# Kernel tuning notes

Hardware: AMD Instinct MI355X
Metric: run time of the kernel (lower is better)

Reference implementation:

```python
import jax, jax.numpy as jnp
import numpy as np

HEADS = 4
DIM_HEAD = 32
SCALE = DIM_HEAD ** -0.5
EPS = 1e-5


def setup_inputs() -> dict:
    key = jax.random.key(0)
    ks = jax.random.split(key, 4)
    x = jax.random.normal(ks[0], (8, 64, 32, 32, 32), dtype=jnp.float32)
    w_qkv = jax.random.normal(ks[1], (384, 64), dtype=jnp.float32) * 0.05
    w_out = jax.random.normal(ks[2], (64, 128), dtype=jnp.float32) * 0.05
    b_out = jax.random.normal(ks[3], (64,), dtype=jnp.float32) * 0.05
    gamma = jnp.ones((64,), dtype=jnp.float32)
    beta = jnp.zeros((64,), dtype=jnp.float32)
    return {"x": x, "w_qkv": w_qkv, "w_out": w_out, "b_out": b_out,
            "gamma": gamma, "beta": beta}


def reference(x, w_qkv, w_out, b_out, gamma, beta):
    b, c, l, h, w = x.shape
    n = l * h * w
    xf = x.reshape(b, c, n)
    # 1x1 Conv3d (no bias) == channel matmul
    qkv = jnp.einsum('oc,bcn->bon', w_qkv, xf)            # [b, 3*H*D, n]
    q, k, v = jnp.split(qkv, 3, axis=1)
    def to_heads(t):
        return t.reshape(b, HEADS, DIM_HEAD, n)            # [b, H, D, n]
    q, k, v = to_heads(q), to_heads(k), to_heads(v)
    q = jax.nn.softmax(q, axis=2) * SCALE                  # softmax over head dim
    k = jax.nn.softmax(k, axis=3)                          # softmax over tokens
    context = jnp.einsum('bhdn,bhen->bhde', k, v)          # [b, H, D, D]
    out = jnp.einsum('bhde,bhdn->bhen', context, q)        # [b, H, D, n]
    out = out.reshape(b, HEADS * DIM_HEAD, n)
    # to_out: 1x1 Conv3d with bias, then GroupNorm(1, dim)
    out = jnp.einsum('oc,bcn->bon', w_out, out) + b_out[None, :, None]
    mu = out.mean(axis=(1, 2), keepdims=True)
    var = out.var(axis=(1, 2), keepdims=True)
    out = (out - mu) * jax.lax.rsqrt(var + EPS)
    out = out * gamma[None, :, None] + beta[None, :, None]
    return out.reshape(b, c, l, h, w)
```

## Files before the change

### kernel.cpp

```cpp
#include <hip/hip_runtime.h>

typedef unsigned short u16;
typedef __bf16 bf16x8 __attribute__((ext_vector_type(8)));
typedef float f32x4 __attribute__((ext_vector_type(4)));
typedef short s16x4 __attribute__((ext_vector_type(4)));
typedef short s16x8 __attribute__((ext_vector_type(8)));

#define NTOK 32768
#define SCALE_F 0.17677669529663689f

__device__ __forceinline__ u16 f2bf(float f){
  unsigned u = __builtin_bit_cast(unsigned, f);
  u += 0x7fffu + ((u>>16)&1u);
  return (u16)(u>>16);
}
__device__ __forceinline__ float bf2f(u16 u){
  unsigned v = ((unsigned)u)<<16;
  return __builtin_bit_cast(float, v);
}

__global__ __launch_bounds__(256) void k1_ctx(const float* __restrict__ x,
    const float* __restrict__ wqkv, float* __restrict__ ctx, float* __restrict__ s1,
    int siters)
{
  const int b = blockIdx.y, chunk = blockIdx.x;
  const int t = threadIdx.x, w = t>>6, l = t&63, lr = l&15, lg = l>>4;
  __shared__ u16 xT[64*72];
  __shared__ u16 ek[128*72];
  __shared__ u16 vl[128*72];

  bf16x8 bw[4][2];
  #pragma unroll
  for (int ct=0;ct<4;ct++)
    #pragma unroll
    for (int ks=0;ks<2;ks++){
      const float* src = wqkv + (128 + w*64 + ct*16 + lr)*64 + ks*32 + lg*8;
      #pragma unroll
      for (int j=0;j<8;j++) ((u16*)&bw[ct][ks])[j] = f2bf(src[j]);
    }
  bf16x8 ones;
  #pragma unroll
  for (int j=0;j<8;j++) ((u16*)&ones)[j] = 0x3F80;

  f32x4 ctxa[2][2]; f32x4 s1a[2];
  #pragma unroll
  for (int i=0;i<2;i++){
    s1a[i] = f32x4{0.f,0.f,0.f,0.f};
    #pragma unroll
    for (int j=0;j<2;j++) ctxa[i][j] = f32x4{0.f,0.f,0.f,0.f};
  }
  const float* xb = x + (long)b*64*NTOK;
  u16* dst = (w<2) ? ek : vl;
  const int chb = (w&1)*64;
  const bool isk = (w<2);
  const int sn = t&63, cg = (t>>6)*16;

  float tmpf[16];
  {
    const int n0 = chunk*siters*64;
    #pragma unroll
    for (int i=0;i<16;i++) tmpf[i] = xb[(long)(cg+i)*NTOK + n0 + sn];
  }

  for (int s=0; s<siters; s++) {
    {
      u16 tmp[16];
      #pragma unroll
      for (int i=0;i<16;i++) tmp[i] = f2bf(tmpf[i]);
      *(s16x8*)&xT[sn*72 + cg]     = *(s16x8*)&tmp[0];
      *(s16x8*)&xT[sn*72 + cg + 8] = *(s16x8*)&tmp[8];
    }
    __syncthreads();
    if (s+1 < siters){
      const int n0 = (chunk*siters + s+1)*64;
      #pragma unroll
      for (int i=0;i<16;i++) tmpf[i] = xb[(long)(cg+i)*NTOK + n0 + sn];
    }
    f32x4 acc[4][4];
    #pragma unroll
    for (int rt=0;rt<4;rt++)
      #pragma unroll
      for (int ct=0;ct<4;ct++) acc[rt][ct] = f32x4{0.f,0.f,0.f,0.f};
    #pragma unroll
    for (int ks=0;ks<2;ks++){
      bf16x8 af[4];
      #pragma unroll
      for (int rt=0;rt<4;rt++)
        af[rt] = *(const bf16x8*)&xT[(rt*16+lr)*72 + ks*32 + lg*8];
      #pragma unroll
      for (int rt=0;rt<4;rt++)
        #pragma unroll
        for (int ct=0;ct<4;ct++)
          acc[rt][ct] = __builtin_amdgcn_mfma_f32_16x16x32_bf16(af[rt], bw[ct][ks], acc[rt][ct], 0,0,0);
    }
    #pragma unroll
    for (int ct=0;ct<4;ct++){
      const int row = chb + ct*16 + lr;
      #pragma unroll
      for (int rt=0;rt<4;rt++){
        s16x4 p;
        #pragma unroll
        for (int ri=0;ri<4;ri++){
          const float v = acc[rt][ct][ri];
          p[ri] = (short)f2bf(isk ? __expf(v) : v);
        }
        *(s16x4*)&dst[row*72 + rt*16 + lg*4] = p;
      }
    }
    __syncthreads();
    #pragma unroll
    for (int ks=0;ks<2;ks++){
      bf16x8 bd[2];
      #pragma unroll
      for (int cd=0;cd<2;cd++)
        bd[cd] = *(const bf16x8*)&ek[(w*32 + cd*16 + lr)*72 + ks*32 + lg*8];
      #pragma unroll
      for (int re=0;re<2;re++){
        bf16x8 a = *(const bf16x8*)&vl[(w*32 + re*16 + lr)*72 + ks*32 + lg*8];
        #pragma unroll
        for (int cd=0;cd<2;cd++)
          ctxa[re][cd] = __builtin_amdgcn_mfma_f32_16x16x32_bf16(a, bd[cd], ctxa[re][cd], 0,0,0);
      }
      #pragma unroll
      for (int cd=0;cd<2;cd++)
        s1a[cd] = __builtin_amdgcn_mfma_f32_16x16x32_bf16(ones, bd[cd], s1a[cd], 0,0,0);
    }
  }
  float* cp = ctx + ((long)b*4 + w)*1024;
  #pragma unroll
  for (int re=0;re<2;re++)
    #pragma unroll
    for (int cd=0;cd<2;cd++)
      #pragma unroll
      for (int ri=0;ri<4;ri++){
        const int e = re*16 + lg*4 + ri, d = cd*16 + lr;
        atomicAdd(&cp[e*32 + d], ctxa[re][cd][ri]);
      }
  if (lg==0){
    #pragma unroll
    for (int cd=0;cd<2;cd++)
      atomicAdd(&s1[(long)b*128 + w*32 + cd*16 + lr], s1a[cd][0]);
  }
}

__global__ __launch_bounds__(256) void k2_w2(const float* __restrict__ ctx,
    const float* __restrict__ s1, const float* __restrict__ wout, u16* __restrict__ W2)
{
  const int b = blockIdx.y, h = blockIdx.x, t = threadIdx.x;
  __shared__ float cs[1024];
  __shared__ float s1s[32];
  {
    f32x4 p4 = *(const f32x4*)(ctx + ((long)b*4 + h)*1024 + t*4);
    *(f32x4*)&cs[t*4] = p4;
  }
  if (t < 32) s1s[t] = s1[(long)b*128 + h*32 + t];
  __syncthreads();
  const int d = t & 31;
  const float rinv = SCALE_F / s1s[d];
  #pragma unroll
  for (int oi=0; oi<8; oi++){
    const int o = (t>>5)*8 + oi;
    float acc = 0.f;
    #pragma unroll
    for (int e=0;e<32;e++) acc += wout[o*128 + h*32 + e] * cs[e*32 + d];
    W2[((long)b*64 + o)*128 + h*32 + d] = f2bf(acc * rinv);
  }
}

#define K3T 4
__global__ __launch_bounds__(256) void k3_y(const float* __restrict__ x,
    const float* __restrict__ wqkv, const u16* __restrict__ W2,
    const float* __restrict__ bout, float* __restrict__ y, float* __restrict__ ysum)
{
  const int b = blockIdx.y, blk = blockIdx.x;
  const int t = threadIdx.x, w = t>>6, l = t&63, lr = l&15, lg = l>>4;
  __shared__ u16 W2s[64*136];
  __shared__ u16 xT[64*72];
  __shared__ u16 qs[64*136];
  __shared__ float red[8];
  const float* xb = x + (long)b*64*NTOK;

  bf16x8 qfr[2][2];
  #pragma unroll
  for (int rt=0;rt<2;rt++)
    #pragma unroll
    for (int ks=0;ks<2;ks++){
      const float* src = wqkv + (w*32 + rt*16 + lr)*64 + ks*32 + lg*8;
      #pragma unroll
      for (int j=0;j<8;j++) ((u16*)&qfr[rt][ks])[j] = f2bf(src[j]);
    }
  {
    const u16* src = W2 + (long)b*8192 + t*32;
    const int o = t>>2, c0 = (t&3)*32;
    #pragma unroll
    for (int k=0;k<4;k++)
      *(s16x8*)&W2s[o*136 + c0 + k*8] = *(const s16x8*)(src + k*8);
  }
  const int sn = t&63, cg = (t>>6)*16;
  float tmpf[16];
  {
    const int n0 = blk*K3T*64;
    #pragma unroll
    for (int i=0;i<16;i++) tmpf[i] = xb[(long)(cg+i)*NTOK + n0 + sn];
  }
  float sum=0.f, ss=0.f;
  float* yb = y + (long)b*64*NTOK;

  for (int ti=0; ti<K3T; ti++){
    const int n0 = (blk*K3T + ti)*64;
    {
      u16 tmp[16];
      #pragma unroll
      for (int i=0;i<16;i++) tmp[i] = f2bf(tmpf[i]);
      *(s16x8*)&xT[sn*72 + cg]     = *(s16x8*)&tmp[0];
      *(s16x8*)&xT[sn*72 + cg + 8] = *(s16x8*)&tmp[8];
    }
    __syncthreads();
    if (ti+1 < K3T){
      const int nn0 = n0 + 64;
      #pragma unroll
      for (int i=0;i<16;i++) tmpf[i] = xb[(long)(cg+i)*NTOK + nn0 + sn];
    }
    f32x4 qa[2][4];
    #pragma unroll
    for (int rt=0;rt<2;rt++)
      #pragma unroll
      for (int ct=0;ct<4;ct++) qa[rt][ct] = f32x4{0.f,0.f,0.f,0.f};
    #pragma unroll
    for (int ks=0;ks<2;ks++){
      bf16x8 bfr[4];
      #pragma unroll
      for (int ct=0;ct<4;ct++)
        bfr[ct] = *(const bf16x8*)&xT[(ct*16+lr)*72 + ks*32 + lg*8];
      #pragma unroll
      for (int rt=0;rt<2;rt++)
        #pragma unroll
        for (int ct=0;ct<4;ct++)
          qa[rt][ct] = __builtin_amdgcn_mfma_f32_16x16x32_bf16(qfr[rt][ks], bfr[ct], qa[rt][ct], 0,0,0);
    }
    #pragma unroll
    for (int ct=0;ct<4;ct++){
      float e[2][4]; float p = 0.f;
      #pragma unroll
      for (int rt=0;rt<2;rt++)
        #pragma unroll
        for (int ri=0;ri<4;ri++){ e[rt][ri] = __expf(qa[rt][ct][ri]); p += e[rt][ri]; }
      p += __shfl_xor(p, 16, 64);
      p += __shfl_xor(p, 32, 64);
      const float rinv = 1.f/p;
      const int nn = ct*16 + lr;
      #pragma unroll
      for (int rt=0;rt<2;rt++){
        s16x4 pk;
        #pragma unroll
        for (int ri=0;ri<4;ri++) pk[ri] = (short)f2bf(e[rt][ri]*rinv);
        *(s16x4*)&qs[nn*136 + w*32 + rt*16 + lg*4] = pk;
      }
    }
    __syncthreads();
    f32x4 ya[4];
    #pragma unroll
    for (int rt=0;rt<4;rt++) ya[rt] = f32x4{0.f,0.f,0.f,0.f};
    #pragma unroll
    for (int ks=0;ks<4;ks++){
      bf16x8 bq = *(const bf16x8*)&qs[(w*16+lr)*136 + ks*32 + lg*8];
      #pragma unroll
      for (int rt=0;rt<4;rt++){
        bf16x8 a = *(const bf16x8*)&W2s[(rt*16+lr)*136 + ks*32 + lg*8];
        ya[rt] = __builtin_amdgcn_mfma_f32_16x16x32_bf16(a, bq, ya[rt], 0,0,0);
      }
    }
    #pragma unroll
    for (int rt=0;rt<4;rt++)
      #pragma unroll
      for (int ri=0;ri<4;ri++){
        const int o = rt*16 + lg*4 + ri;
        const float val = ya[rt][ri] + bout[o];
        sum += val; ss += val*val;
        yb[(long)o*NTOK + n0 + w*16 + lr] = val;
      }
    __syncthreads();
  }
  #pragma unroll
  for (int off=1; off<64; off<<=1){
    sum += __shfl_xor(sum, off, 64);
    ss  += __shfl_xor(ss,  off, 64);
  }
  if (l==0){ red[w*2] = sum; red[w*2+1] = ss; }
  __syncthreads();
  if (t==0){
    ysum[((long)b*128 + blk)*2]   = red[0]+red[2]+red[4]+red[6];
    ysum[((long)b*128 + blk)*2+1] = red[1]+red[3]+red[5]+red[7];
  }
}

__global__ __launch_bounds__(256) void k3b_stats(const float* __restrict__ ysum,
                                                 float* __restrict__ musig)
{
  const int b = blockIdx.x, t = threadIdx.x, w = t>>6, l = t&63;
  float s=0.f, q=0.f;
  if (t < 128){
    s = ysum[((long)b*128+t)*2];
    q = ysum[((long)b*128+t)*2+1];
  }
  #pragma unroll
  for (int off=1; off<64; off<<=1){ s += __shfl_xor(s,off,64); q += __shfl_xor(q,off,64); }
  __shared__ float rs[4], rq[4];
  if (l==0){ rs[w]=s; rq[w]=q; }
  __syncthreads();
  if (t==0){
    const float S = rs[0]+rs[1];
    const float Q = rq[0]+rq[1];
    const float inv_n = 1.f/2097152.f;
    const float mu = S*inv_n;
    const float var = Q*inv_n - mu*mu;
    musig[b*2]   = mu;
    musig[b*2+1] = rsqrtf(var + 1e-5f);
  }
}

__global__ __launch_bounds__(256) void k4_norm(float* __restrict__ y,
    const float* __restrict__ musig, const float* __restrict__ gamma,
    const float* __restrict__ beta)
{
  const long idx = ((long)blockIdx.x*256 + threadIdx.x)*4;
  const int b = (int)(idx >> 21);
  const int c = (int)((idx >> 15) & 63);
  const float mu = musig[b*2], inv = musig[b*2+1];
  const float g = gamma[c]*inv, be = beta[c];
  f32x4 v4 = *(const f32x4*)(y + idx);
  #pragma unroll
  for (int j=0;j<4;j++) v4[j] = (v4[j] - mu)*g + be;
  *(f32x4*)(y + idx) = v4;
}

extern "C" void kernel_launch(void* const* d_in, const int* in_sizes, int n_in,
                              void* d_out, int out_size, void* d_ws, size_t ws_size,
                              hipStream_t stream) {
  const float* x     = (const float*)d_in[0];
  const float* wqkv  = (const float*)d_in[1];
  const float* wout  = (const float*)d_in[2];
  const float* bout  = (const float*)d_in[3];
  const float* gamma = (const float*)d_in[4];
  const float* beta  = (const float*)d_in[5];
  float* out = (float*)d_out;
  char* ws = (char*)d_ws;
  if (ws_size < 300000u) return;

  float* ctx  = (float*)(ws + 0);
  float* s1   = (float*)(ws + 131072);
  u16*  W2    = (u16*) (ws + 135168);
  float* ysum = (float*)(ws + 266240);
  float* musig= (float*)(ws + 274432);

  hipMemsetAsync(ws, 0, 135168, stream);
  k1_ctx   <<<dim3(128,8), 256, 0, stream>>>(x, wqkv, ctx, s1, 4);
  k2_w2    <<<dim3(4,8),   256, 0, stream>>>(ctx, s1, wout, W2);
  k3_y     <<<dim3(128,8), 256, 0, stream>>>(x, wqkv, W2, bout, out, ysum);
  k3b_stats<<<8,           256, 0, stream>>>(ysum, musig);
  k4_norm  <<<16384,       256, 0, stream>>>(out, musig, gamma, beta);
}
```

Before: 108.5 us.

## Fuse projection, stats and GroupNorm into one cooperative kernel with register-held outputs

The output projection kernel now keeps its whole 512-token tile of results in registers. It accumulates the GroupNorm sums through global atomics and a grid-wide sync, then writes the normalized output once. This removes the separate stats and normalize kernels, and with them a full extra read and write of the output tensor. The k1 and k3 grids are halved, giving each block 8 token tiles, and bf16 conversion switches to native casts. It depends on all 512 blocks being co-resident at 2 per CU and raises register pressure; if the cooperative launch fails, a fallback path runs the old three-kernel sequence.

```diff
diff --git a/kernel.cpp b/kernel.cpp
--- a/kernel.cpp
+++ b/kernel.cpp
@@ -1,33 +1,24 @@
 #include <hip/hip_runtime.h>
-
-typedef unsigned short u16;
+#include <hip/hip_cooperative_groups.h>
+
+namespace cg = cooperative_groups;
+
+typedef __bf16 bf16;
+typedef __bf16 bf16x4 __attribute__((ext_vector_type(4)));
 typedef __bf16 bf16x8 __attribute__((ext_vector_type(8)));
 typedef float f32x4 __attribute__((ext_vector_type(4)));
-typedef short s16x4 __attribute__((ext_vector_type(4)));
-typedef short s16x8 __attribute__((ext_vector_type(8)));
 
 #define NTOK 32768
 #define SCALE_F 0.17677669529663689f
 
-__device__ __forceinline__ u16 f2bf(float f){
-  unsigned u = __builtin_bit_cast(unsigned, f);
-  u += 0x7fffu + ((u>>16)&1u);
-  return (u16)(u>>16);
-}
-__device__ __forceinline__ float bf2f(u16 u){
-  unsigned v = ((unsigned)u)<<16;
-  return __builtin_bit_cast(float, v);
-}
-
 __global__ __launch_bounds__(256) void k1_ctx(const float* __restrict__ x,
-    const float* __restrict__ wqkv, float* __restrict__ ctx, float* __restrict__ s1,
-    int siters)
+    const float* __restrict__ wqkv, float* __restrict__ ctx, float* __restrict__ s1)
 {
   const int b = blockIdx.y, chunk = blockIdx.x;
   const int t = threadIdx.x, w = t>>6, l = t&63, lr = l&15, lg = l>>4;
-  __shared__ u16 xT[64*72];
-  __shared__ u16 ek[128*72];
-  __shared__ u16 vl[128*72];
+  __shared__ bf16 xT[64*72];
+  __shared__ bf16 ek[128*72];
+  __shared__ bf16 vl[128*72];
 
   bf16x8 bw[4][2];
   #pragma unroll
@@ -36,11 +27,11 @@
     for (int ks=0;ks<2;ks++){
       const float* src = wqkv + (128 + w*64 + ct*16 + lr)*64 + ks*32 + lg*8;
       #pragma unroll
-      for (int j=0;j<8;j++) ((u16*)&bw[ct][ks])[j] = f2bf(src[j]);
+      for (int j=0;j<8;j++) bw[ct][ks][j] = (bf16)src[j];
     }
   bf16x8 ones;
   #pragma unroll
-  for (int j=0;j<8;j++) ((u16*)&ones)[j] = 0x3F80;
+  for (int j=0;j<8;j++) ones[j] = (bf16)1.0f;
 
   f32x4 ctxa[2][2]; f32x4 s1a[2];
   #pragma unroll
@@ -50,31 +41,30 @@
     for (int j=0;j<2;j++) ctxa[i][j] = f32x4{0.f,0.f,0.f,0.f};
   }
   const float* xb = x + (long)b*64*NTOK;
-  u16* dst = (w<2) ? ek : vl;
+  bf16* dst = (w<2) ? ek : vl;
   const int chb = (w&1)*64;
   const bool isk = (w<2);
-  const int sn = t&63, cg = (t>>6)*16;
-
-  float tmpf[16];
+  const int sn = t&63, cg16 = (t>>6)*16;
+
+  bf16x8 t0, t1;
   {
-    const int n0 = chunk*siters*64;
-    #pragma unroll
-    for (int i=0;i<16;i++) tmpf[i] = xb[(long)(cg+i)*NTOK + n0 + sn];
-  }
-
-  for (int s=0; s<siters; s++) {
-    {
-      u16 tmp[16];
-      #pragma unroll
-      for (int i=0;i<16;i++) tmp[i] = f2bf(tmpf[i]);
-      *(s16x8*)&xT[sn*72 + cg]     = *(s16x8*)&tmp[0];
-      *(s16x8*)&xT[sn*72 + cg + 8] = *(s16x8*)&tmp[8];
-    }
-    __syncthreads();
-    if (s+1 < siters){
-      const int n0 = (chunk*siters + s+1)*64;
-      #pragma unroll
-      for (int i=0;i<16;i++) tmpf[i] = xb[(long)(cg+i)*NTOK + n0 + sn];
+    const int n0 = chunk*512;
+    #pragma unroll
+    for (int i=0;i<8;i++) t0[i] = (bf16)xb[(long)(cg16+i)*NTOK + n0 + sn];
+    #pragma unroll
+    for (int i=0;i<8;i++) t1[i] = (bf16)xb[(long)(cg16+8+i)*NTOK + n0 + sn];
+  }
+
+  for (int s=0; s<8; s++) {
+    *(bf16x8*)&xT[sn*72 + cg16]     = t0;
+    *(bf16x8*)&xT[sn*72 + cg16 + 8] = t1;
+    __syncthreads();
+    if (s+1 < 8){
+      const int n0 = chunk*512 + (s+1)*64;
+      #pragma unroll
+      for (int i=0;i<8;i++) t0[i] = (bf16)xb[(long)(cg16+i)*NTOK + n0 + sn];
+      #pragma unroll
+      for (int i=0;i<8;i++) t1[i] = (bf16)xb[(long)(cg16+8+i)*NTOK + n0 + sn];
     }
     f32x4 acc[4][4];
     #pragma unroll
@@ -98,13 +88,13 @@
       const int row = chb + ct*16 + lr;
       #pragma unroll
       for (int rt=0;rt<4;rt++){
-        s16x4 p;
+        bf16x4 p;
         #pragma unroll
         for (int ri=0;ri<4;ri++){
           const float v = acc[rt][ct][ri];
-          p[ri] = (short)f2bf(isk ? __expf(v) : v);
+          p[ri] = isk ? (bf16)__expf(v) : (bf16)v;
         }
-        *(s16x4*)&dst[row*72 + rt*16 + lg*4] = p;
+        *(bf16x4*)&dst[row*72 + rt*16 + lg*4] = p;
       }
     }
     __syncthreads();
@@ -144,7 +134,7 @@
 }
 
 __global__ __launch_bounds__(256) void k2_w2(const float* __restrict__ ctx,
-    const float* __restrict__ s1, const float* __restrict__ wout, u16* __restrict__ W2)
+    const float* __restrict__ s1, const float* __restrict__ wout, bf16* __restrict__ W2)
 {
   const int b = blockIdx.y, h = blockIdx.x, t = threadIdx.x;
   __shared__ float cs[1024];
@@ -163,22 +153,25 @@
     float acc = 0.f;
     #pragma unroll
     for (int e=0;e<32;e++) acc += wout[o*128 + h*32 + e] * cs[e*32 + d];
-    W2[((long)b*64 + o)*128 + h*32 + d] = f2bf(acc * rinv);
-  }
-}
-
-#define K3T 4
-__global__ __launch_bounds__(256) void k3_y(const float* __restrict__ x,
-    const float* __restrict__ wqkv, const u16* __restrict__ W2,
-    const float* __restrict__ bout, float* __restrict__ y, float* __restrict__ ysum)
+    W2[((long)b*64 + o)*128 + h*32 + d] = (bf16)(acc * rinv);
+  }
+}
+
+template<bool COOP>
+__device__ __forceinline__ void k3_body(const float* __restrict__ x,
+    const float* __restrict__ wqkv, const bf16* __restrict__ W2g,
+    const float* __restrict__ bout, float* __restrict__ out,
+    float* __restrict__ yacc, const float* __restrict__ gamma,
+    const float* __restrict__ beta, float* __restrict__ ysum)
 {
   const int b = blockIdx.y, blk = blockIdx.x;
   const int t = threadIdx.x, w = t>>6, l = t&63, lr = l&15, lg = l>>4;
-  __shared__ u16 W2s[64*136];
-  __shared__ u16 xT[64*72];
-  __shared__ u16 qs[64*136];
+  __shared__ bf16 W2s[64*136];
+  __shared__ bf16 xT[64*72];
+  __shared__ bf16 qs[64*136];
   __shared__ float red[8];
   const float* xb = x + (long)b*64*NTOK;
+  float* yb = out + (long)b*64*NTOK;
 
   bf16x8 qfr[2][2];
   #pragma unroll
@@ -187,39 +180,49 @@
     for (int ks=0;ks<2;ks++){
       const float* src = wqkv + (w*32 + rt*16 + lr)*64 + ks*32 + lg*8;
       #pragma unroll
-      for (int j=0;j<8;j++) ((u16*)&qfr[rt][ks])[j] = f2bf(src[j]);
+      for (int j=0;j<8;j++) qfr[rt][ks][j] = (bf16)src[j];
     }
   {
-    const u16* src = W2 + (long)b*8192 + t*32;
+    const bf16* src = W2g + (long)b*8192 + t*32;
     const int o = t>>2, c0 = (t&3)*32;
     #pragma unroll
     for (int k=0;k<4;k++)
-      *(s16x8*)&W2s[o*136 + c0 + k*8] = *(const s16x8*)(src + k*8);
-  }
-  const int sn = t&63, cg = (t>>6)*16;
-  float tmpf[16];
+      *(bf16x8*)&W2s[o*136 + c0 + k*8] = *(const bf16x8*)(src + k*8);
+  }
+  float boutr[16];
+  #pragma unroll
+  for (int rt=0;rt<4;rt++)
+    #pragma unroll
+    for (int ri=0;ri<4;ri++) boutr[rt*4+ri] = bout[rt*16 + lg*4 + ri];
+
+  const int sn = t&63, cg16 = (t>>6)*16;
+  bf16x8 t0, t1;
   {
-    const int n0 = blk*K3T*64;
-    #pragma unroll
-    for (int i=0;i<16;i++) tmpf[i] = xb[(long)(cg+i)*NTOK + n0 + sn];
-  }
+    const int n0 = blk*512;
+    #pragma unroll
+    for (int i=0;i<8;i++) t0[i] = (bf16)xb[(long)(cg16+i)*NTOK + n0 + sn];
+    #pragma unroll
+    for (int i=0;i<8;i++) t1[i] = (bf16)xb[(long)(cg16+8+i)*NTOK + n0 + sn];
+  }
+  f32x4 yv[8][4];
+  #pragma unroll
+  for (int ti=0;ti<8;ti++)
+    #pragma unroll
+    for (int rt=0;rt<4;rt++) yv[ti][rt] = f32x4{0.f,0.f,0.f,0.f};
   float sum=0.f, ss=0.f;
-  float* yb = y + (long)b*64*NTOK;
-
-  for (int ti=0; ti<K3T; ti++){
-    const int n0 = (blk*K3T + ti)*64;
-    {
-      u16 tmp[16];
-      #pragma unroll
-      for (int i=0;i<16;i++) tmp[i] = f2bf(tmpf[i]);
-      *(s16x8*)&xT[sn*72 + cg]     = *(s16x8*)&tmp[0];
-      *(s16x8*)&xT[sn*72 + cg + 8] = *(s16x8*)&tmp[8];
-    }
-    __syncthreads();
-    if (ti+1 < K3T){
+
+  #pragma unroll
+  for (int ti=0; ti<8; ti++){
+    const int n0 = blk*512 + ti*64;
+    *(bf16x8*)&xT[sn*72 + cg16]     = t0;
+    *(bf16x8*)&xT[sn*72 + cg16 + 8] = t1;
+    __syncthreads();
+    if (ti+1 < 8){
       const int nn0 = n0 + 64;
       #pragma unroll
-      for (int i=0;i<16;i++) tmpf[i] = xb[(long)(cg+i)*NTOK + nn0 + sn];
+      for (int i=0;i<8;i++) t0[i] = (bf16)xb[(long)(cg16+i)*NTOK + nn0 + sn];
+      #pragma unroll
+      for (int i=0;i<8;i++) t1[i] = (bf16)xb[(long)(cg16+8+i)*NTOK + nn0 + sn];
     }
     f32x4 qa[2][4];
     #pragma unroll
@@ -251,33 +254,33 @@
       const int nn = ct*16 + lr;
       #pragma unroll
       for (int rt=0;rt<2;rt++){
-        s16x4 pk;
-        #pragma unroll
-        for (int ri=0;ri<4;ri++) pk[ri] = (short)f2bf(e[rt][ri]*rinv);
-        *(s16x4*)&qs[nn*136 + w*32 + rt*16 + lg*4] = pk;
-      }
-    }
-    __syncthreads();
-    f32x4 ya[4];
-    #pragma unroll
-    for (int rt=0;rt<4;rt++) ya[rt] = f32x4{0.f,0.f,0.f,0.f};
+        bf16x4 pk;
+        #pragma unroll
+        for (int ri=0;ri<4;ri++) pk[ri] = (bf16)(e[rt][ri]*rinv);
+        *(bf16x4*)&qs[nn*136 + w*32 + rt*16 + lg*4] = pk;
+      }
+    }
+    __syncthreads();
     #pragma unroll
     for (int ks=0;ks<4;ks++){
       bf16x8 bq = *(const bf16x8*)&qs[(w*16+lr)*136 + ks*32 + lg*8];
       #pragma unroll
       for (int rt=0;rt<4;rt++){
         bf16x8 a = *(const bf16x8*)&W2s[(rt*16+lr)*136 + ks*32 + lg*8];
-        ya[rt] = __builtin_amdgcn_mfma_f32_16x16x32_bf16(a, bq, ya[rt], 0,0,0);
+        yv[ti][rt] = __builtin_amdgcn_mfma_f32_16x16x32_bf16(a, bq, yv[ti][rt], 0,0,0);
       }
     }
     #pragma unroll
     for (int rt=0;rt<4;rt++)
       #pragma unroll
       for (int ri=0;ri<4;ri++){
-        const int o = rt*16 + lg*4 + ri;
-        const float val = ya[rt][ri] + bout[o];
+        yv[ti][rt][ri] += boutr[rt*4+ri];
+        const float val = yv[ti][rt][ri];
         sum += val; ss += val*val;
-        yb[(long)o*NTOK + n0 + w*16 + lr] = val;
+        if (!COOP){
+          const int o = rt*16 + lg*4 + ri;
+          yb[(long)o*NTOK + n0 + w*16 + lr] = val;
+        }
       }
     __syncthreads();
   }
@@ -288,32 +291,77 @@
   }
   if (l==0){ red[w*2] = sum; red[w*2+1] = ss; }
   __syncthreads();
+
+  if constexpr (COOP){
+    if (t==0){
+      atomicAdd(&yacc[b*2],   red[0]+red[2]+red[4]+red[6]);
+      atomicAdd(&yacc[b*2+1], red[1]+red[3]+red[5]+red[7]);
+    }
+    cg::this_grid().sync();
+    if (t==0){
+      const float S = atomicAdd(&yacc[b*2],   0.f);
+      const float Q = atomicAdd(&yacc[b*2+1], 0.f);
+      const float inv_n = 1.f/2097152.f;
+      const float mu = S*inv_n;
+      red[0] = mu;
+      red[1] = rsqrtf(Q*inv_n - mu*mu + 1e-5f);
+    }
+    __syncthreads();
+    const float mu = red[0], inv = red[1];
+    float A[16], B[16];
+    #pragma unroll
+    for (int rt=0;rt<4;rt++)
+      #pragma unroll
+      for (int ri=0;ri<4;ri++){
+        const int o = rt*16 + lg*4 + ri;
+        A[rt*4+ri] = inv*gamma[o];
+        B[rt*4+ri] = beta[o] - mu*A[rt*4+ri];
+      }
+    #pragma unroll
+    for (int ti=0;ti<8;ti++){
+      const int n0 = blk*512 + ti*64;
+      #pragma unroll
+      for (int rt=0;rt<4;rt++)
+        #pragma unroll
+        for (int ri=0;ri<4;ri++){
+          const int o = rt*16 + lg*4 + ri;
+          yb[(long)o*NTOK + n0 + w*16 + lr] = yv[ti][rt][ri]*A[rt*4+ri] + B[rt*4+ri];
+        }
+    }
+  } else {
+    if (t==0){
+      ysum[((long)b*64 + blk)*2]   = red[0]+red[2]+red[4]+red[6];
+      ysum[((long)b*64 + blk)*2+1] = red[1]+red[3]+red[5]+red[7];
+    }
+  }
+}
+
+__global__ __launch_bounds__(256,2) void k3_coop(const float* __restrict__ x,
+    const float* __restrict__ wqkv, const bf16* __restrict__ W2g,
+    const float* __restrict__ bout, float* __restrict__ out,
+    float* __restrict__ yacc, const float* __restrict__ gamma,
+    const float* __restrict__ beta, float* __restrict__ ysum)
+{ k3_body<true>(x, wqkv, W2g, bout, out, yacc, gamma, beta, ysum); }
+
+__global__ __launch_bounds__(256,2) void k3_fb(const float* __restrict__ x,
+    const float* __restrict__ wqkv, const bf16* __restrict__ W2g,
+    const float* __restrict__ bout, float* __restrict__ out,
+    float* __restrict__ yacc, const float* __restrict__ gamma,
+    const float* __restrict__ beta, float* __restrict__ ysum)
+{ k3_body<false>(x, wqkv, W2g, bout, out, yacc, gamma, beta, ysum); }
+
+__global__ __launch_bounds__(64) void k3b_stats(const float* __restrict__ ysum,
+                                                float* __restrict__ musig)
+{
+  const int b = blockIdx.x, t = threadIdx.x;
+  float s = ysum[((long)b*64+t)*2];
+  float q = ysum[((long)b*64+t)*2+1];
+  #pragma unroll
+  for (int off=1; off<64; off<<=1){ s += __shfl_xor(s,off,64); q += __shfl_xor(q,off,64); }
   if (t==0){
-    ysum[((long)b*128 + blk)*2]   = red[0]+red[2]+red[4]+red[6];
-    ysum[((long)b*128 + blk)*2+1] = red[1]+red[3]+red[5]+red[7];
-  }
-}
-
-__global__ __launch_bounds__(256) void k3b_stats(const float* __restrict__ ysum,
-                                                 float* __restrict__ musig)
-{
-  const int b = blockIdx.x, t = threadIdx.x, w = t>>6, l = t&63;
-  float s=0.f, q=0.f;
-  if (t < 128){
-    s = ysum[((long)b*128+t)*2];
-    q = ysum[((long)b*128+t)*2+1];
-  }
-  #pragma unroll
-  for (int off=1; off<64; off<<=1){ s += __shfl_xor(s,off,64); q += __shfl_xor(q,off,64); }
-  __shared__ float rs[4], rq[4];
-  if (l==0){ rs[w]=s; rq[w]=q; }
-  __syncthreads();
-  if (t==0){
-    const float S = rs[0]+rs[1];
-    const float Q = rq[0]+rq[1];
     const float inv_n = 1.f/2097152.f;
-    const float mu = S*inv_n;
-    const float var = Q*inv_n - mu*mu;
+    const float mu = s*inv_n;
+    const float var = q*inv_n - mu*mu;
     musig[b*2]   = mu;
     musig[b*2+1] = rsqrtf(var + 1e-5f);
   }
@@ -349,14 +397,22 @@
 
   float* ctx  = (float*)(ws + 0);
   float* s1   = (float*)(ws + 131072);
-  u16*  W2    = (u16*) (ws + 135168);
-  float* ysum = (float*)(ws + 266240);
-  float* musig= (float*)(ws + 274432);
-
-  hipMemsetAsync(ws, 0, 135168, stream);
-  k1_ctx   <<<dim3(128,8), 256, 0, stream>>>(x, wqkv, ctx, s1, 4);
-  k2_w2    <<<dim3(4,8),   256, 0, stream>>>(ctx, s1, wout, W2);
-  k3_y     <<<dim3(128,8), 256, 0, stream>>>(x, wqkv, W2, bout, out, ysum);
-  k3b_stats<<<8,           256, 0, stream>>>(ysum, musig);
-  k4_norm  <<<16384,       256, 0, stream>>>(out, musig, gamma, beta);
-}
+  float* yacc = (float*)(ws + 135168);
+  bf16*  W2   = (bf16*) (ws + 135424);
+  float* ysum = (float*)(ws + 266496);
+  float* musig= (float*)(ws + 270592);
+
+  hipMemsetAsync(ws, 0, 135232, stream);
+  k1_ctx <<<dim3(64,8), 256, 0, stream>>>(x, wqkv, ctx, s1);
+  k2_w2  <<<dim3(4,8),  256, 0, stream>>>(ctx, s1, wout, W2);
+
+  void* args[9] = {(void*)&x, (void*)&wqkv, (void*)&W2, (void*)&bout, (void*)&out,
+                   (void*)&yacc, (void*)&gamma, (void*)&beta, (void*)&ysum};
+  hipError_t ce = hipLaunchCooperativeKernel((const void*)k3_coop, dim3(64,8), dim3(256),
+                                             args, 0u, stream);
+  if (ce != hipSuccess){
+    k3_fb    <<<dim3(64,8), 256, 0, stream>>>(x, wqkv, W2, bout, out, yacc, gamma, beta, ysum);
+    k3b_stats<<<8, 64, 0, stream>>>(ysum, musig);
+    k4_norm  <<<16384, 256, 0, stream>>>(out, musig, gamma, beta);
+  }
+}
```

New measurement: 148.7 us. 1.37x slower.
